# Kernel tuning notes

Measured on AMD Instinct MI355X. Metric: run time of the kernel, lower is better.

Reference implementation:

```python
import jax, jax.numpy as jnp
import numpy as np

B, C, H, W = 4, 128, 64, 64
NUM_HEADS = 4
HEAD_DIM = C // NUM_HEADS


def setup_inputs() -> dict:
    key = jax.random.key(0)
    ks = jax.random.split(key, 9)
    s = 0.02
    return {
        "x": jax.random.normal(ks[0], (B, C, H, W), dtype=jnp.float32),
        "wq": jax.random.normal(ks[1], (C, C), dtype=jnp.float32) * s,
        "bq": jax.random.normal(ks[2], (C,), dtype=jnp.float32) * s,
        "wk": jax.random.normal(ks[3], (C, C), dtype=jnp.float32) * s,
        "bk": jax.random.normal(ks[4], (C,), dtype=jnp.float32) * s,
        "wv": jax.random.normal(ks[5], (C, C), dtype=jnp.float32) * s,
        "bv": jax.random.normal(ks[6], (C,), dtype=jnp.float32) * s,
        "wo": jax.random.normal(ks[7], (C, C), dtype=jnp.float32) * s,
        "bo": jax.random.normal(ks[8], (C,), dtype=jnp.float32) * s,
    }


def _proj(w, b, xf):
    # 1x1 conv == channel-mixing linear: xf is (B, C, N)
    return jnp.einsum("oc,bcn->bon", w, xf) + b[None, :, None]


def reference(x, wq, bq, wk, bk, wv, bv, wo, bo):
    b, c, h, w = x.shape
    n = h * w
    nh, hd = NUM_HEADS, HEAD_DIM
    xf = x.reshape(b, c, n)
    q = _proj(wq, bq, xf).reshape(b, nh, hd, n)
    k = _proj(wk, bk, xf).reshape(b, nh, hd, n)
    v = _proj(wv, bv, xf).reshape(b, nh, hd, n)
    # scores: (b, heads, n, n)
    scores = jnp.einsum("bhdn,bhdm->bhnm", q, k) / jnp.sqrt(jnp.float32(hd)).astype(x.dtype)
    prob = jax.nn.softmax(scores, axis=-1)
    # attn_out: (b, heads, head_dim, n)
    attn = jnp.einsum("bhnm,bhdm->bhdn", prob, v).reshape(b, c, n)
    out = _proj(wo, bo, attn).reshape(b, c, h, w)
    return x + out
```

## Files before the change

kernel.cpp:

```cpp
#include <hip/hip_runtime.h>
#include <hip/hip_bf16.h>

#define BB 4
#define CC 128
#define NN 4096
#define NHEAD 4
#define HDIM 32
#define KSPLIT 4

typedef short bf16x8_t __attribute__((ext_vector_type(8)));
typedef float f32x4_t __attribute__((ext_vector_type(4)));
typedef int i32x4_t __attribute__((ext_vector_type(4)));

#define MFMA16(a, b, c) __builtin_amdgcn_mfma_f32_16x16x32_bf16(a, b, c, 0, 0, 0)
#define EXP2(x) __builtin_amdgcn_exp2f(x)

#define QSCALE (0.17677669529663687f * 1.4426950408889634f)

static __device__ inline unsigned short f2bf(float f) {
  unsigned u = __builtin_bit_cast(unsigned, f);
  u += 0x7fffu + ((u >> 16) & 1u);
  return (unsigned short)(u >> 16);
}
static __device__ inline unsigned pk2(float lo, float hi) {
  return (unsigned)f2bf(lo) | ((unsigned)f2bf(hi) << 16);
}
static __device__ inline unsigned pack_trunc(float lo, float hi) {
  return __builtin_amdgcn_perm(__builtin_bit_cast(unsigned, hi),
                               __builtin_bit_cast(unsigned, lo), 0x07060302u);
}
static __device__ inline float bfu_lo(unsigned v) {
  return __builtin_bit_cast(float, v << 16);
}
static __device__ inline float bfu_hi(unsigned v) {
  return __builtin_bit_cast(float, v & 0xFFFF0000u);
}

static __device__ inline void gload_lds16(const unsigned short* gsrc, void* ldst) {
  __builtin_amdgcn_global_load_lds(
      (const __attribute__((address_space(1))) unsigned int*)gsrc,
      (__attribute__((address_space(3))) unsigned int*)ldst, 16, 0, 0);
}

static __device__ inline void waitcnt_vm0() {
  asm volatile("s_waitcnt vmcnt(0)" ::: "memory");
}

__global__ __launch_bounds__(256) void wconv_kernel(
    const float* __restrict__ wq, const float* __restrict__ wk,
    const float* __restrict__ wv, const float* __restrict__ wo,
    unsigned short* __restrict__ wb) {
  int f = (blockIdx.x * 256 + threadIdx.x) * 8;
  int m = f >> 14, off = f & 16383;
  const float* src = (m == 0) ? wq : (m == 1) ? wk : (m == 2) ? wv : wo;
  float sc = (m == 0) ? QSCALE : 1.0f;
  float4 a = *(const float4*)(src + off);
  float4 b = *(const float4*)(src + off + 4);
  ushort4 u0, u1;
  u0.x = f2bf(a.x * sc); u0.y = f2bf(a.y * sc); u0.z = f2bf(a.z * sc); u0.w = f2bf(a.w * sc);
  u1.x = f2bf(b.x * sc); u1.y = f2bf(b.y * sc); u1.z = f2bf(b.z * sc); u1.w = f2bf(b.w * sc);
  *(ushort4*)(wb + f) = u0;
  *(ushort4*)(wb + f + 4) = u1;
}

__global__ __launch_bounds__(256) void qkv_mfma_kernel(
    const float* __restrict__ x,
    const unsigned short* __restrict__ wqb, const unsigned short* __restrict__ wkb,
    const unsigned short* __restrict__ wvb,
    const float* __restrict__ bq, const float* __restrict__ bk,
    const float* __restrict__ bv,
    unsigned short* __restrict__ qt, unsigned short* __restrict__ kt,
    unsigned short* __restrict__ vg) {
  __shared__ __attribute__((aligned(16))) unsigned short xsb[64][136];
  __shared__ unsigned short vt[64][66];
  const int b = blockIdx.y, nt = blockIdx.x;
  const int proj = blockIdx.z >> 1, half = blockIdx.z & 1;
  const int tid = threadIdx.x;

#pragma unroll
  for (int i = 0; i < 8; i++) {
    int f = tid + 256 * i;
    int c = f >> 4, n4 = (f & 15) * 4;
    float4 v4 = *(const float4*)(x + ((size_t)b * CC + c) * NN + nt * 64 + n4);
    xsb[n4 + 0][c] = f2bf(v4.x);
    xsb[n4 + 1][c] = f2bf(v4.y);
    xsb[n4 + 2][c] = f2bf(v4.z);
    xsb[n4 + 3][c] = f2bf(v4.w);
  }
  __syncthreads();

  const int lane = tid & 63, w = tid >> 6;
  const int l16 = lane & 15, g = lane >> 4;
  const int nl = w * 16;
  const int ngl = nt * 64 + nl;

  bf16x8_t xf[4];
#pragma unroll
  for (int ks = 0; ks < 4; ks++)
    xf[ks] = *(const bf16x8_t*)&xsb[nl + l16][ks * 32 + g * 8];

  const unsigned short* wm = (proj == 0) ? wqb : (proj == 1) ? wkb : wvb;
  const float* bias = (proj == 0) ? bq : (proj == 1) ? bk : bv;
  const float bsc = (proj == 0) ? QSCALE : 1.0f;
  unsigned short* qkdst = proj ? kt : qt;

#pragma unroll
  for (int i = 0; i < 4; i++) {
    const int ot = half * 4 + i;
    f32x4_t acc;
#pragma unroll
    for (int r = 0; r < 4; r++) acc[r] = bias[ot * 16 + g * 4 + r] * bsc;
#pragma unroll
    for (int ks = 0; ks < 4; ks++) {
      bf16x8_t wf = *(const bf16x8_t*)(wm + (size_t)(ot * 16 + l16) * CC + ks * 32 + g * 8);
      acc = MFMA16(wf, xf[ks], acc);
    }
    if (proj < 2) {
      unsigned p0 = pk2(acc[0], acc[1]);
      unsigned p1 = pk2(acc[2], acc[3]);
      unsigned q0 = (unsigned)__shfl_xor((int)p0, 16);
      unsigned q1 = (unsigned)__shfl_xor((int)p1, 16);
      if ((g & 1) == 0) {
        int hh = ot >> 1, dblk = (ot & 1) * 2 + (g >> 1);
        unsigned short* dst =
            qkdst + (((size_t)(b * NHEAD + hh) * 4 + dblk) * NN + ngl + l16) * 8;
        uint4 val = make_uint4(p0, p1, q0, q1);
        *(uint4*)dst = val;
      }
    } else {
#pragma unroll
      for (int r = 0; r < 4; r++) vt[i * 16 + g * 4 + r][nl + l16] = f2bf(acc[r]);
    }
  }

  if (proj == 2) {
    __syncthreads();
#pragma unroll
    for (int c = 0; c < 2; c++) {
      int cid = c * 256 + tid;
      int hh_l = cid >> 8, inner = cid & 255;
      int hh = half * 2 + hh_l;
      int g2 = inner & 3, l16v = (inner >> 2) & 15, fh = inner >> 6;
      int fv = fh >> 1, halfv = fh & 1;
      int o_l = hh_l * 32 + halfv * 16 + l16v;
      int n0 = fv * 32 + g2 * 4;
      unsigned d0 = *(const unsigned*)&vt[o_l][n0];
      unsigned d1 = *(const unsigned*)&vt[o_l][n0 + 2];
      unsigned d2 = *(const unsigned*)&vt[o_l][n0 + 16];
      unsigned d3 = *(const unsigned*)&vt[o_l][n0 + 18];
      uint4 val = make_uint4(d0, d1, d2, d3);
      *(uint4*)(vg + (((size_t)(b * NHEAD + hh) * 64 + nt) * 256 + inner) * 8) = val;
    }
  }
}

__global__ __launch_bounds__(256, 4) void attn_mfma6_kernel(
    const unsigned short* __restrict__ qt, const unsigned short* __restrict__ kt,
    const unsigned short* __restrict__ vg,
    unsigned* __restrict__ obf, float* __restrict__ lpart) {
  __shared__ __attribute__((aligned(16))) unsigned short smem[2][4096];

  const int chunk = blockIdx.x & (KSPLIT - 1), nt = blockIdx.x / KSPLIT;
  const int h = blockIdx.y, b = blockIdx.z;
  const int bh = b * NHEAD + h;
  const int tid = threadIdx.x, lane = tid & 63, wid = tid >> 6;
  const int l16 = lane & 15, g = lane >> 4;
  const int nbase = nt * 128 + wid * 32;

  const unsigned short* qb = qt + (size_t)bh * NN * HDIM;
  const unsigned short* kb = kt + (size_t)bh * NN * HDIM;
  const unsigned short* vgb = vg + (size_t)bh * 64 * 2048;

  const bf16x8_t qf0 = *(const bf16x8_t*)(qb + ((size_t)g * NN + nbase + l16) * 8);
  const bf16x8_t qf1 = *(const bf16x8_t*)(qb + ((size_t)g * NN + nbase + 16 + l16) * 8);

  f32x4_t o00 = {0, 0, 0, 0}, o01 = {0, 0, 0, 0};
  f32x4_t o10 = {0, 0, 0, 0}, o11 = {0, 0, 0, 0};
  float lA = 0.f, lB = 0.f;
  const f32x4_t zf = {0, 0, 0, 0};

  const int NITER = 64 / KSPLIT;
  const int mt0 = chunk * NITER;

  const unsigned short* ksrc = kb + ((size_t)g * NN + mt0 * 64 + wid * 16 + l16) * 8;
  const unsigned short* vsrc = vgb + (size_t)mt0 * 2048 + (size_t)((wid * 16 + l16) * 4 + g) * 8;

  auto stage = [&](int p, int i) {
    gload_lds16(ksrc + (size_t)i * 512, &smem[p][wid * 512]);
    gload_lds16(vsrc + (size_t)i * 2048, &smem[p][2048 + wid * 512]);
  };

  auto body = [&](int p) {
    const unsigned short* sk = &smem[p][0];
    bf16x8_t k0 = *(const bf16x8_t*)(sk + 0 * 512 + lane * 8);
    bf16x8_t k1 = *(const bf16x8_t*)(sk + 1 * 512 + lane * 8);
    bf16x8_t k2 = *(const bf16x8_t*)(sk + 2 * 512 + lane * 8);
    bf16x8_t k3 = *(const bf16x8_t*)(sk + 3 * 512 + lane * 8);
    bf16x8_t vf0 = *(const bf16x8_t*)(sk + 2048 + 0 * 512 + lane * 8);
    bf16x8_t vf2 = *(const bf16x8_t*)(sk + 2048 + 1 * 512 + lane * 8);
    bf16x8_t vf1 = *(const bf16x8_t*)(sk + 2048 + 2 * 512 + lane * 8);
    bf16x8_t vf3 = *(const bf16x8_t*)(sk + 2048 + 3 * 512 + lane * 8);

    f32x4_t sA0 = MFMA16(k0, qf0, zf), sA1 = MFMA16(k1, qf0, zf);
    f32x4_t sA2 = MFMA16(k2, qf0, zf), sA3 = MFMA16(k3, qf0, zf);
    f32x4_t sB0 = MFMA16(k0, qf1, zf), sB1 = MFMA16(k1, qf1, zf);
    f32x4_t sB2 = MFMA16(k2, qf1, zf), sB3 = MFMA16(k3, qf1, zf);

#pragma unroll
    for (int r = 0; r < 4; r++) {
      sA0[r] = EXP2(sA0[r]); sA1[r] = EXP2(sA1[r]);
      sA2[r] = EXP2(sA2[r]); sA3[r] = EXP2(sA3[r]);
      sB0[r] = EXP2(sB0[r]); sB1[r] = EXP2(sB1[r]);
      sB2[r] = EXP2(sB2[r]); sB3[r] = EXP2(sB3[r]);
      lA += (sA0[r] + sA1[r]) + (sA2[r] + sA3[r]);
      lB += (sB0[r] + sB1[r]) + (sB2[r] + sB3[r]);
    }

    i32x4_t pA0i = {(int)pack_trunc(sA0[0], sA0[1]), (int)pack_trunc(sA0[2], sA0[3]),
                    (int)pack_trunc(sA1[0], sA1[1]), (int)pack_trunc(sA1[2], sA1[3])};
    i32x4_t pA1i = {(int)pack_trunc(sA2[0], sA2[1]), (int)pack_trunc(sA2[2], sA2[3]),
                    (int)pack_trunc(sA3[0], sA3[1]), (int)pack_trunc(sA3[2], sA3[3])};
    i32x4_t pB0i = {(int)pack_trunc(sB0[0], sB0[1]), (int)pack_trunc(sB0[2], sB0[3]),
                    (int)pack_trunc(sB1[0], sB1[1]), (int)pack_trunc(sB1[2], sB1[3])};
    i32x4_t pB1i = {(int)pack_trunc(sB2[0], sB2[1]), (int)pack_trunc(sB2[2], sB2[3]),
                    (int)pack_trunc(sB3[0], sB3[1]), (int)pack_trunc(sB3[2], sB3[3])};
    bf16x8_t pA0 = __builtin_bit_cast(bf16x8_t, pA0i);
    bf16x8_t pA1 = __builtin_bit_cast(bf16x8_t, pA1i);
    bf16x8_t pB0 = __builtin_bit_cast(bf16x8_t, pB0i);
    bf16x8_t pB1 = __builtin_bit_cast(bf16x8_t, pB1i);

    o00 = MFMA16(vf0, pA0, o00); o00 = MFMA16(vf1, pA1, o00);
    o01 = MFMA16(vf2, pA0, o01); o01 = MFMA16(vf3, pA1, o01);
    o10 = MFMA16(vf0, pB0, o10); o10 = MFMA16(vf1, pB1, o10);
    o11 = MFMA16(vf2, pB0, o11); o11 = MFMA16(vf3, pB1, o11);
  };

  stage(0, 0);
  waitcnt_vm0();
  __syncthreads();
  for (int mi = 0; mi < NITER; mi += 2) {
    stage(1, mi + 1);
    body(0);
    waitcnt_vm0();
    __syncthreads();
    if (mi + 2 < NITER) stage(0, mi + 2);
    body(1);
    waitcnt_vm0();
    __syncthreads();
  }

  lA += __shfl_xor(lA, 16); lA += __shfl_xor(lA, 32);
  lB += __shfl_xor(lB, 16); lB += __shfl_xor(lB, 32);

  unsigned* ob = obf + (size_t)(chunk * BB * NHEAD + bh) * 32 * 2048;
  const int dw = (nbase >> 1) + l16;
#pragma unroll
  for (int r = 0; r < 4; r++) {
    ob[(size_t)(g * 4 + r) * 2048 + dw] = pk2(o00[r], o10[r]);
    ob[(size_t)(16 + g * 4 + r) * 2048 + dw] = pk2(o01[r], o11[r]);
  }
  if (g == 0) {
    float* lb_ = lpart + (size_t)(chunk * BB * NHEAD + bh) * NN;
    lb_[nbase + l16] = lA;
    lb_[nbase + 16 + l16] = lB;
  }
}

__global__ __launch_bounds__(256) void combine_kernel(
    const unsigned* __restrict__ obf, const float* __restrict__ lpart,
    unsigned short* __restrict__ attnT) {
  const int dw = blockIdx.x * 256 + threadIdx.x;
  const int bh = blockIdx.y, dg = blockIdx.z;
  const int b = bh >> 2, h = bh & 3;
  const int n0 = ((dw >> 4) << 5) + (dw & 15), n1 = n0 + 16;

  float l0 = 0.f, l1 = 0.f;
#pragma unroll
  for (int c = 0; c < KSPLIT; c++) {
    const float* lp = lpart + (size_t)(c * BB * NHEAD + bh) * NN;
    l0 += lp[n0];
    l1 += lp[n1];
  }
  float inv0 = 1.f / l0, inv1 = 1.f / l1;

  float s0[8], s1[8];
#pragma unroll
  for (int j = 0; j < 8; j++) { s0[j] = 0.f; s1[j] = 0.f; }
#pragma unroll
  for (int c = 0; c < KSPLIT; c++) {
    const unsigned* ob =
        obf + (size_t)(c * BB * NHEAD + bh) * 32 * 2048 + (size_t)dg * 8 * 2048 + dw;
#pragma unroll
    for (int j = 0; j < 8; j++) {
      unsigned v = ob[(size_t)j * 2048];
      s0[j] += bfu_lo(v);
      s1[j] += bfu_hi(v);
    }
  }
  unsigned w0[4], w1[4];
#pragma unroll
  for (int p = 0; p < 4; p++) {
    w0[p] = pk2(s0[2 * p] * inv0, s0[2 * p + 1] * inv0);
    w1[p] = pk2(s1[2 * p] * inv1, s1[2 * p + 1] * inv1);
  }
  unsigned short* d0 = attnT + ((size_t)b * NN + n0) * CC + h * HDIM + dg * 8;
  unsigned short* d1 = attnT + ((size_t)b * NN + n1) * CC + h * HDIM + dg * 8;
  *(uint4*)d0 = *(uint4*)&w0[0];
  *(uint4*)d1 = *(uint4*)&w1[0];
}

__global__ __launch_bounds__(256) void out_mfma_kernel(
    const unsigned short* __restrict__ attnT, const unsigned short* __restrict__ wob,
    const float* __restrict__ bo, const float* __restrict__ x,
    float* __restrict__ out) {
  const int b = blockIdx.y, nt = blockIdx.x, quarter = blockIdx.z;
  const int tid = threadIdx.x, lane = tid & 63, w = tid >> 6;
  const int l16 = lane & 15, g = lane >> 4;
  const int n0 = nt * 64 + w * 16;

  bf16x8_t bf[4];
#pragma unroll
  for (int ks = 0; ks < 4; ks++)
    bf[ks] = *(const bf16x8_t*)(attnT + ((size_t)b * NN + n0 + l16) * CC + ks * 32 + g * 8);

#pragma unroll
  for (int mi = 0; mi < 2; mi++) {
    int mt = quarter * 2 + mi;
    f32x4_t acc;
#pragma unroll
    for (int r = 0; r < 4; r++) acc[r] = bo[mt * 16 + g * 4 + r];
#pragma unroll
    for (int ks = 0; ks < 4; ks++) {
      bf16x8_t af = *(const bf16x8_t*)(wob + (size_t)(mt * 16 + l16) * CC + ks * 32 + g * 8);
      acc = MFMA16(af, bf[ks], acc);
    }
#pragma unroll
    for (int r = 0; r < 4; r++) {
      int o = mt * 16 + g * 4 + r;
      size_t addr = ((size_t)b * CC + o) * NN + n0 + l16;
      out[addr] = acc[r] + x[addr];
    }
  }
}

extern "C" void kernel_launch(void* const* d_in, const int* in_sizes, int n_in,
                              void* d_out, int out_size, void* d_ws, size_t ws_size,
                              hipStream_t stream) {
  const float* x  = (const float*)d_in[0];
  const float* wq = (const float*)d_in[1];
  const float* bq = (const float*)d_in[2];
  const float* wk = (const float*)d_in[3];
  const float* bk = (const float*)d_in[4];
  const float* wv = (const float*)d_in[5];
  const float* bv = (const float*)d_in[6];
  const float* wo = (const float*)d_in[7];
  const float* bo = (const float*)d_in[8];
  float* out = (float*)d_out;

  char* w = (char*)d_ws;
  const size_t SZ = (size_t)BB * NHEAD * NN * HDIM * 2;
  unsigned short* qt    = (unsigned short*)w;
  unsigned short* kt    = (unsigned short*)(w + SZ);
  unsigned short* vg    = (unsigned short*)(w + 2 * SZ);
  unsigned short* wb    = (unsigned short*)(w + 3 * SZ);
  unsigned* obf = (unsigned*)(w + 3 * SZ + 131072);
  float* lpart = (float*)(w + 3 * SZ + 131072 +
                          (size_t)KSPLIT * BB * NHEAD * HDIM * NN * 2);
  unsigned short* attnT = qt;
  unsigned short* wqb = wb, *wkb = wb + 16384, *wvb = wb + 32768, *wob = wb + 49152;

  wconv_kernel<<<32, 256, 0, stream>>>(wq, wk, wv, wo, wb);
  qkv_mfma_kernel<<<dim3(NN / 64, BB, 6), 256, 0, stream>>>(
      x, wqb, wkb, wvb, bq, bk, bv, qt, kt, vg);
  attn_mfma6_kernel<<<dim3((NN / 128) * KSPLIT, NHEAD, BB), 256, 0, stream>>>(
      qt, kt, vg, obf, lpart);
  combine_kernel<<<dim3(8, BB * NHEAD, 4), 256, 0, stream>>>(obf, lpart, attnT);
  out_mfma_kernel<<<dim3(NN / 64, BB, 4), 256, 0, stream>>>(attnT, wob, bo, x, out);
}
```

Baseline: 150.3 us.

## Fuse weight conversion, combine and output projection; compute softmax sums with MFMA

Removes the separate weight-conversion kernel by converting fp32 weights to bf16 inline inside the QKV and output projection kernels. Merges the split-K combine and output projection into one kernel that normalises partial outputs into LDS and runs the output MFMA directly, so the attnT round trip through global memory goes away. In the attention kernel, the softmax row sums are computed with extra MFMAs against a ones matrix instead of scalar adds and shuffles. This cuts two launches and some memory traffic, at the cost of redundant weight conversion in every block and extra MFMA work in the attention loop.

```diff
diff --git a/kernel.cpp b/kernel.cpp
--- a/kernel.cpp
+++ b/kernel.cpp
@@ -36,6 +36,14 @@
   return __builtin_bit_cast(float, v & 0xFFFF0000u);
 }
 
+static __device__ inline bf16x8_t wfrag_f32(const float* __restrict__ Wp, float sc) {
+  float4 a = *(const float4*)(Wp);
+  float4 b = *(const float4*)(Wp + 4);
+  i32x4_t pi = {(int)pk2(a.x * sc, a.y * sc), (int)pk2(a.z * sc, a.w * sc),
+                (int)pk2(b.x * sc, b.y * sc), (int)pk2(b.z * sc, b.w * sc)};
+  return __builtin_bit_cast(bf16x8_t, pi);
+}
+
 static __device__ inline void gload_lds16(const unsigned short* gsrc, void* ldst) {
   __builtin_amdgcn_global_load_lds(
       (const __attribute__((address_space(1))) unsigned int*)gsrc,
@@ -46,27 +54,10 @@
   asm volatile("s_waitcnt vmcnt(0)" ::: "memory");
 }
 
-__global__ __launch_bounds__(256) void wconv_kernel(
-    const float* __restrict__ wq, const float* __restrict__ wk,
-    const float* __restrict__ wv, const float* __restrict__ wo,
-    unsigned short* __restrict__ wb) {
-  int f = (blockIdx.x * 256 + threadIdx.x) * 8;
-  int m = f >> 14, off = f & 16383;
-  const float* src = (m == 0) ? wq : (m == 1) ? wk : (m == 2) ? wv : wo;
-  float sc = (m == 0) ? QSCALE : 1.0f;
-  float4 a = *(const float4*)(src + off);
-  float4 b = *(const float4*)(src + off + 4);
-  ushort4 u0, u1;
-  u0.x = f2bf(a.x * sc); u0.y = f2bf(a.y * sc); u0.z = f2bf(a.z * sc); u0.w = f2bf(a.w * sc);
-  u1.x = f2bf(b.x * sc); u1.y = f2bf(b.y * sc); u1.z = f2bf(b.z * sc); u1.w = f2bf(b.w * sc);
-  *(ushort4*)(wb + f) = u0;
-  *(ushort4*)(wb + f + 4) = u1;
-}
-
 __global__ __launch_bounds__(256) void qkv_mfma_kernel(
     const float* __restrict__ x,
-    const unsigned short* __restrict__ wqb, const unsigned short* __restrict__ wkb,
-    const unsigned short* __restrict__ wvb,
+    const float* __restrict__ wq, const float* __restrict__ wk,
+    const float* __restrict__ wv,
     const float* __restrict__ bq, const float* __restrict__ bk,
     const float* __restrict__ bv,
     unsigned short* __restrict__ qt, unsigned short* __restrict__ kt,
@@ -99,7 +90,7 @@
   for (int ks = 0; ks < 4; ks++)
     xf[ks] = *(const bf16x8_t*)&xsb[nl + l16][ks * 32 + g * 8];
 
-  const unsigned short* wm = (proj == 0) ? wqb : (proj == 1) ? wkb : wvb;
+  const float* wm = (proj == 0) ? wq : (proj == 1) ? wk : wv;
   const float* bias = (proj == 0) ? bq : (proj == 1) ? bk : bv;
   const float bsc = (proj == 0) ? QSCALE : 1.0f;
   unsigned short* qkdst = proj ? kt : qt;
@@ -112,7 +103,7 @@
     for (int r = 0; r < 4; r++) acc[r] = bias[ot * 16 + g * 4 + r] * bsc;
 #pragma unroll
     for (int ks = 0; ks < 4; ks++) {
-      bf16x8_t wf = *(const bf16x8_t*)(wm + (size_t)(ot * 16 + l16) * CC + ks * 32 + g * 8);
+      bf16x8_t wf = wfrag_f32(wm + (size_t)(ot * 16 + l16) * CC + ks * 32 + g * 8, bsc);
       acc = MFMA16(wf, xf[ks], acc);
     }
     if (proj < 2) {
@@ -154,7 +145,7 @@
   }
 }
 
-__global__ __launch_bounds__(256, 4) void attn_mfma6_kernel(
+__global__ __launch_bounds__(256, 4) void attn_mfma7_kernel(
     const unsigned short* __restrict__ qt, const unsigned short* __restrict__ kt,
     const unsigned short* __restrict__ vg,
     unsigned* __restrict__ obf, float* __restrict__ lpart) {
@@ -176,8 +167,10 @@
 
   f32x4_t o00 = {0, 0, 0, 0}, o01 = {0, 0, 0, 0};
   f32x4_t o10 = {0, 0, 0, 0}, o11 = {0, 0, 0, 0};
-  float lA = 0.f, lB = 0.f;
+  f32x4_t la = {0, 0, 0, 0}, lb = {0, 0, 0, 0};
   const f32x4_t zf = {0, 0, 0, 0};
+  const i32x4_t onesi = {0x3F803F80, 0x3F803F80, 0x3F803F80, 0x3F803F80};
+  const bf16x8_t ones = __builtin_bit_cast(bf16x8_t, onesi);
 
   const int NITER = 64 / KSPLIT;
   const int mt0 = chunk * NITER;
@@ -212,8 +205,6 @@
       sA2[r] = EXP2(sA2[r]); sA3[r] = EXP2(sA3[r]);
       sB0[r] = EXP2(sB0[r]); sB1[r] = EXP2(sB1[r]);
       sB2[r] = EXP2(sB2[r]); sB3[r] = EXP2(sB3[r]);
-      lA += (sA0[r] + sA1[r]) + (sA2[r] + sA3[r]);
-      lB += (sB0[r] + sB1[r]) + (sB2[r] + sB3[r]);
     }
 
     i32x4_t pA0i = {(int)pack_trunc(sA0[0], sA0[1]), (int)pack_trunc(sA0[2], sA0[3]),
@@ -233,6 +224,9 @@
     o01 = MFMA16(vf2, pA0, o01); o01 = MFMA16(vf3, pA1, o01);
     o10 = MFMA16(vf0, pB0, o10); o10 = MFMA16(vf1, pB1, o10);
     o11 = MFMA16(vf2, pB0, o11); o11 = MFMA16(vf3, pB1, o11);
+
+    la = MFMA16(ones, pA0, la); la = MFMA16(ones, pA1, la);
+    lb = MFMA16(ones, pB0, lb); lb = MFMA16(ones, pB1, lb);
   };
 
   stage(0, 0);
@@ -249,9 +243,6 @@
     __syncthreads();
   }
 
-  lA += __shfl_xor(lA, 16); lA += __shfl_xor(lA, 32);
-  lB += __shfl_xor(lB, 16); lB += __shfl_xor(lB, 32);
-
   unsigned* ob = obf + (size_t)(chunk * BB * NHEAD + bh) * 32 * 2048;
   const int dw = (nbase >> 1) + l16;
 #pragma unroll
@@ -261,84 +252,68 @@
   }
   if (g == 0) {
     float* lb_ = lpart + (size_t)(chunk * BB * NHEAD + bh) * NN;
-    lb_[nbase + l16] = lA;
-    lb_[nbase + 16 + l16] = lB;
-  }
-}
-
-__global__ __launch_bounds__(256) void combine_kernel(
+    lb_[nbase + l16] = la[0];
+    lb_[nbase + 16 + l16] = lb[0];
+  }
+}
+
+__global__ __launch_bounds__(256) void outc_kernel(
     const unsigned* __restrict__ obf, const float* __restrict__ lpart,
-    unsigned short* __restrict__ attnT) {
-  const int dw = blockIdx.x * 256 + threadIdx.x;
-  const int bh = blockIdx.y, dg = blockIdx.z;
-  const int b = bh >> 2, h = bh & 3;
-  const int n0 = ((dw >> 4) << 5) + (dw & 15), n1 = n0 + 16;
-
-  float l0 = 0.f, l1 = 0.f;
-#pragma unroll
-  for (int c = 0; c < KSPLIT; c++) {
-    const float* lp = lpart + (size_t)(c * BB * NHEAD + bh) * NN;
-    l0 += lp[n0];
-    l1 += lp[n1];
-  }
-  float inv0 = 1.f / l0, inv1 = 1.f / l1;
-
-  float s0[8], s1[8];
-#pragma unroll
-  for (int j = 0; j < 8; j++) { s0[j] = 0.f; s1[j] = 0.f; }
-#pragma unroll
-  for (int c = 0; c < KSPLIT; c++) {
-    const unsigned* ob =
-        obf + (size_t)(c * BB * NHEAD + bh) * 32 * 2048 + (size_t)dg * 8 * 2048 + dw;
+    const float* __restrict__ wo, const float* __restrict__ bo,
+    const float* __restrict__ x, float* __restrict__ out) {
+  __shared__ __attribute__((aligned(16))) unsigned short asb[32][136];
+  const int b = blockIdx.y, nt2 = blockIdx.x;
+  const int nb = nt2 * 32, dwb = nt2 * 16;
+  const int tid = threadIdx.x, lane = tid & 63;
+  const int wv = tid >> 6, l16 = lane & 15, g = lane >> 4;
+
+  {
+    float l0 = 0.f, l1 = 0.f;
+#pragma unroll
+    for (int c = 0; c < KSPLIT; c++) {
+      const float* lp = lpart + (size_t)(c * BB * NHEAD + b * NHEAD + wv) * NN + nb;
+      l0 += lp[l16];
+      l1 += lp[16 + l16];
+    }
+    float inv0 = 1.f / l0, inv1 = 1.f / l1;
 #pragma unroll
     for (int j = 0; j < 8; j++) {
-      unsigned v = ob[(size_t)j * 2048];
-      s0[j] += bfu_lo(v);
-      s1[j] += bfu_hi(v);
-    }
-  }
-  unsigned w0[4], w1[4];
-#pragma unroll
-  for (int p = 0; p < 4; p++) {
-    w0[p] = pk2(s0[2 * p] * inv0, s0[2 * p + 1] * inv0);
-    w1[p] = pk2(s1[2 * p] * inv1, s1[2 * p + 1] * inv1);
-  }
-  unsigned short* d0 = attnT + ((size_t)b * NN + n0) * CC + h * HDIM + dg * 8;
-  unsigned short* d1 = attnT + ((size_t)b * NN + n1) * CC + h * HDIM + dg * 8;
-  *(uint4*)d0 = *(uint4*)&w0[0];
-  *(uint4*)d1 = *(uint4*)&w1[0];
-}
-
-__global__ __launch_bounds__(256) void out_mfma_kernel(
-    const unsigned short* __restrict__ attnT, const unsigned short* __restrict__ wob,
-    const float* __restrict__ bo, const float* __restrict__ x,
-    float* __restrict__ out) {
-  const int b = blockIdx.y, nt = blockIdx.x, quarter = blockIdx.z;
-  const int tid = threadIdx.x, lane = tid & 63, w = tid >> 6;
-  const int l16 = lane & 15, g = lane >> 4;
-  const int n0 = nt * 64 + w * 16;
-
-  bf16x8_t bf[4];
-#pragma unroll
-  for (int ks = 0; ks < 4; ks++)
-    bf[ks] = *(const bf16x8_t*)(attnT + ((size_t)b * NN + n0 + l16) * CC + ks * 32 + g * 8);
-
-#pragma unroll
-  for (int mi = 0; mi < 2; mi++) {
-    int mt = quarter * 2 + mi;
-    f32x4_t acc;
-#pragma unroll
-    for (int r = 0; r < 4; r++) acc[r] = bo[mt * 16 + g * 4 + r];
+      int d = g * 8 + j;
+      float s0 = 0.f, s1 = 0.f;
+#pragma unroll
+      for (int c = 0; c < KSPLIT; c++) {
+        unsigned v = obf[(size_t)(c * BB * NHEAD + b * NHEAD + wv) * 65536 +
+                         (size_t)d * 2048 + dwb + l16];
+        s0 += bfu_lo(v);
+        s1 += bfu_hi(v);
+      }
+      int cfull = wv * 32 + d;
+      asb[l16][cfull] = f2bf(s0 * inv0);
+      asb[16 + l16][cfull] = f2bf(s1 * inv1);
+    }
+  }
+  __syncthreads();
+
+#pragma unroll
+  for (int oi = 0; oi < 2; oi++) {
+    const int ot = wv * 2 + oi;
+    f32x4_t a0, a1;
+#pragma unroll
+    for (int r = 0; r < 4; r++) { a0[r] = bo[ot * 16 + g * 4 + r]; a1[r] = a0[r]; }
 #pragma unroll
     for (int ks = 0; ks < 4; ks++) {
-      bf16x8_t af = *(const bf16x8_t*)(wob + (size_t)(mt * 16 + l16) * CC + ks * 32 + g * 8);
-      acc = MFMA16(af, bf[ks], acc);
+      bf16x8_t af = wfrag_f32(wo + (size_t)(ot * 16 + l16) * CC + ks * 32 + g * 8, 1.0f);
+      bf16x8_t b0 = *(const bf16x8_t*)&asb[l16][ks * 32 + g * 8];
+      bf16x8_t b1 = *(const bf16x8_t*)&asb[16 + l16][ks * 32 + g * 8];
+      a0 = MFMA16(af, b0, a0);
+      a1 = MFMA16(af, b1, a1);
     }
 #pragma unroll
     for (int r = 0; r < 4; r++) {
-      int o = mt * 16 + g * 4 + r;
-      size_t addr = ((size_t)b * CC + o) * NN + n0 + l16;
-      out[addr] = acc[r] + x[addr];
+      int o = ot * 16 + g * 4 + r;
+      size_t ad = ((size_t)b * CC + o) * NN + nb + l16;
+      out[ad] = a0[r] + x[ad];
+      out[ad + 16] = a1[r] + x[ad + 16];
     }
   }
 }
@@ -359,21 +334,16 @@
 
   char* w = (char*)d_ws;
   const size_t SZ = (size_t)BB * NHEAD * NN * HDIM * 2;
-  unsigned short* qt    = (unsigned short*)w;
-  unsigned short* kt    = (unsigned short*)(w + SZ);
-  unsigned short* vg    = (unsigned short*)(w + 2 * SZ);
-  unsigned short* wb    = (unsigned short*)(w + 3 * SZ);
-  unsigned* obf = (unsigned*)(w + 3 * SZ + 131072);
-  float* lpart = (float*)(w + 3 * SZ + 131072 +
+  unsigned short* qt = (unsigned short*)w;
+  unsigned short* kt = (unsigned short*)(w + SZ);
+  unsigned short* vg = (unsigned short*)(w + 2 * SZ);
+  unsigned* obf = (unsigned*)(w + 3 * SZ);
+  float* lpart = (float*)(w + 3 * SZ +
                           (size_t)KSPLIT * BB * NHEAD * HDIM * NN * 2);
-  unsigned short* attnT = qt;
-  unsigned short* wqb = wb, *wkb = wb + 16384, *wvb = wb + 32768, *wob = wb + 49152;
-
-  wconv_kernel<<<32, 256, 0, stream>>>(wq, wk, wv, wo, wb);
+
   qkv_mfma_kernel<<<dim3(NN / 64, BB, 6), 256, 0, stream>>>(
-      x, wqb, wkb, wvb, bq, bk, bv, qt, kt, vg);
-  attn_mfma6_kernel<<<dim3((NN / 128) * KSPLIT, NHEAD, BB), 256, 0, stream>>>(
+      x, wq, wk, wv, bq, bk, bv, qt, kt, vg);
+  attn_mfma7_kernel<<<dim3((NN / 128) * KSPLIT, NHEAD, BB), 256, 0, stream>>>(
       qt, kt, vg, obf, lpart);
-  combine_kernel<<<dim3(8, BB * NHEAD, 4), 256, 0, stream>>>(obf, lpart, attnT);
-  out_mfma_kernel<<<dim3(NN / 64, BB, 4), 256, 0, stream>>>(attnT, wob, bo, x, out);
-}
+  outc_kernel<<<dim3(NN / 32, BB), 256, 0, stream>>>(obf, lpart, wo, bo, x, out);
+}
```

Result: no change. 149.4 us (-0.6%).
